# Performance work log

Hardware: AMD Instinct MI355X
Metric: run time of the kernel (lower is better)

The kernel has to match this reference:

```python
import jax, jax.numpy as jnp
import numpy as np

EMBED_DIM = 1024
NUM_HEADS = 16
HEAD_DIM = EMBED_DIM // NUM_HEADS


def setup_inputs() -> dict:
    key = jax.random.key(0)
    k1, k2, k3, k4 = jax.random.split(key, 4)
    B, N, D = 4, 2048, EMBED_DIM
    x = jax.random.normal(k1, (B, N, D), dtype=jnp.float32)
    # torch nn.Linear layout: weight [out_features, in_features]
    w_qkv = jax.random.normal(k2, (3 * D, D), dtype=jnp.float32) * (1.0 / np.sqrt(D))
    w_out = jax.random.normal(k3, (D, D), dtype=jnp.float32) * (1.0 / np.sqrt(D))
    b_out = jax.random.normal(k4, (D,), dtype=jnp.float32) * 0.01
    return {"x": x, "w_qkv": w_qkv, "w_out": w_out, "b_out": b_out}


def reference(x, w_qkv, w_out, b_out):
    B, N, D = x.shape
    H, Hd = NUM_HEADS, HEAD_DIM
    qkv = (x @ w_qkv.T).reshape(B, N, 3, H, Hd)
    q, k, v = qkv[:, :, 0], qkv[:, :, 1], qkv[:, :, 2]  # [B,N,H,Hd]
    # NOTE: contracts over BOTH heads and head_dim -> single shared [B,N,N] map
    scores = jnp.einsum('bnhd,bmhd->bnm', q, k) / np.sqrt(Hd).astype(np.float32)
    attn = jax.nn.softmax(scores, axis=-1)
    out = jnp.einsum('bnm,bmhd->bnhd', attn, v).reshape(B, N, D)
    return out @ w_out.T + b_out
```

## Files before the change

kernel.cpp:

```cpp
#include <hip/hip_runtime.h>


typedef __bf16 bf16;
typedef __attribute__((ext_vector_type(8))) __bf16 bf16x8;
typedef __attribute__((ext_vector_type(4))) __bf16 bf16x4;
typedef __attribute__((ext_vector_type(16))) float f32x16;

#define BATCH 4
#define NTOK  2048
#define DIM   1024
#define MROWS (BATCH * NTOK)
#define QKVC  (3 * DIM)

__device__ __forceinline__ void async16(const bf16* g, bf16* l) {
  __builtin_amdgcn_global_load_lds(
      (const __attribute__((address_space(1))) void*)g,
      (__attribute__((address_space(3))) void*)l, 16, 0, 0);
}

__device__ __forceinline__ void cvt4(const float* in, bf16* out, int i4) {
  float4 f = *(const float4*)(in + i4 * 4);
  bf16x4 o;
  o.x = (bf16)f.x; o.y = (bf16)f.y; o.z = (bf16)f.z; o.w = (bf16)f.w;
  *(bf16x4*)(out + i4 * 4) = o;
}

__global__ void prep(const float* __restrict__ x, const float* __restrict__ wqkv,
                     const float* __restrict__ wout,
                     bf16* __restrict__ Xbf, bf16* __restrict__ Wqkvb,
                     bf16* __restrict__ Woutb, float* __restrict__ L) {
  const int nx = MROWS * DIM / 4, nq = QKVC * DIM / 4, nw = DIM * DIM / 4;
  const int nl = BATCH * NTOK / 4;
  int i = blockIdx.x * blockDim.x + threadIdx.x;
  if (i < nx) cvt4(x, Xbf, i);
  else if (i < nx + nq) cvt4(wqkv, Wqkvb, i - nx);
  else if (i < nx + nq + nw) cvt4(wout, Woutb, i - nx - nq);
  else if (i < nx + nq + nw + nl) {
    float4 z = {0.f, 0.f, 0.f, 0.f};
    *(float4*)(L + (i - nx - nq - nw) * 4) = z;
  }
}

struct GemmCore {
  const bf16 *ga[4], *gb[4];
  int sIdx[4];
  int wm, wn, l31, half;
};

__device__ __forceinline__ GemmCore gemm_setup(const bf16* A, const bf16* Bm,
                                               int lda, int ldb,
                                               long rowA, long rowB) {
  GemmCore g;
  const int tid = threadIdx.x;
  const int wave = tid >> 6, lane = tid & 63;
  g.wm = (wave >> 1) << 6;
  g.wn = (wave & 1) << 6;
  g.l31 = lane & 31;
  g.half = lane >> 5;
  const int srow = tid >> 3;
  const int sc   = tid & 7;
  const int scol = (sc ^ (srow & 7)) << 3;
#pragma unroll
  for (int seg = 0; seg < 4; ++seg) {
    g.ga[seg] = A  + (rowA + srow + 32 * seg) * (long)lda + scol;
    g.gb[seg] = Bm + (rowB + srow + 32 * seg) * (long)ldb + scol;
    g.sIdx[seg] = (srow + 32 * seg) * 64 + sc * 8;
  }
  return g;
}

__device__ __forceinline__ void gemm_kloop(const GemmCore& g, int K,
                                           bf16* As, bf16* Bs, f32x16 acc[2][2]) {
  const int sw = g.l31 & 7;
  for (int kt = 0; kt < K; kt += 64) {
#pragma unroll
    for (int seg = 0; seg < 4; ++seg) {
      async16(g.ga[seg] + kt, As + g.sIdx[seg]);
      async16(g.gb[seg] + kt, Bs + g.sIdx[seg]);
    }
    __syncthreads();

    bf16x8 af[2][4], bfm[2][4];
#pragma unroll
    for (int ti = 0; ti < 2; ++ti)
#pragma unroll
      for (int s = 0; s < 4; ++s)
        af[ti][s] = *(const bf16x8*)&As[(g.wm + ti * 32 + g.l31) * 64 + ((s * 2 + g.half) ^ sw) * 8];
#pragma unroll
    for (int tj = 0; tj < 2; ++tj)
#pragma unroll
      for (int s = 0; s < 4; ++s)
        bfm[tj][s] = *(const bf16x8*)&Bs[(g.wn + tj * 32 + g.l31) * 64 + ((s * 2 + g.half) ^ sw) * 8];

#pragma unroll
    for (int s = 0; s < 4; ++s)
#pragma unroll
      for (int ti = 0; ti < 2; ++ti)
#pragma unroll
        for (int tj = 0; tj < 2; ++tj)
          acc[ti][tj] = __builtin_amdgcn_mfma_f32_32x32x16_bf16(
              af[ti][s], bfm[tj][s], acc[ti][tj], 0, 0, 0);

    __syncthreads();
  }
}

__launch_bounds__(256)
__global__ void gemm_qkv(const bf16* __restrict__ Xb, const bf16* __restrict__ Wq,
                         bf16* __restrict__ QKV) {
  __shared__ alignas(16) bf16 As[128 * 64];
  __shared__ alignas(16) bf16 Bs[128 * 64];
  int wg = blockIdx.x;
  wg = (wg & 7) * 192 + (wg >> 3);
  const int by = wg / 24, bx = wg - by * 24;

  const long rowA = (long)by * 128;
  const long rowB = (long)bx * 128;
  GemmCore g = gemm_setup(Xb, Wq, DIM, DIM, rowA, rowB);
  f32x16 acc[2][2] = {};
  gemm_kloop(g, DIM, As, Bs, acc);

#pragma unroll
  for (int ti = 0; ti < 2; ++ti)
#pragma unroll
    for (int tj = 0; tj < 2; ++tj) {
      const long col = rowB + g.wn + tj * 32 + g.l31;
#pragma unroll
      for (int r = 0; r < 16; ++r) {
        const long row = rowA + g.wm + ti * 32 + (r & 3) + 8 * (r >> 2) + 4 * g.half;
        QKV[row * (long)QKVC + col] = (bf16)acc[ti][tj][r];
      }
    }
}

__launch_bounds__(256)
__global__ void gemm_sv(const bf16* __restrict__ QKV, const bf16* __restrict__ Wout,
                        bf16* __restrict__ E, bf16* __restrict__ Vpp,
                        float* __restrict__ Lroot) {
  __shared__ alignas(16) bf16 As[128 * 64];
  __shared__ alignas(16) bf16 Bs[128 * 64];
  int wg = blockIdx.x;
  wg = (wg & 7) * 192 + (wg >> 3);

  if (wg < 1024) {
    const int z = wg >> 8, rem = wg & 255;
    const int by = rem >> 4, bx = rem & 15;
    const bf16* A  = QKV + (long)z * NTOK * QKVC;
    const bf16* Bm = A + DIM;
    const long rowA = (long)by * 128;
    const long rowB = (long)bx * 128;
    GemmCore g = gemm_setup(A, Bm, QKVC, QKVC, rowA, rowB);
    f32x16 acc[2][2] = {};
    gemm_kloop(g, DIM, As, Bs, acc);

    bf16* C = E + (long)z * NTOK * NTOK;
    float* L = Lroot + (long)z * NTOK;
#pragma unroll
    for (int ti = 0; ti < 2; ++ti) {
#pragma unroll
      for (int r = 0; r < 16; ++r) {
        const long row = rowA + g.wm + ti * 32 + (r & 3) + 8 * (r >> 2) + 4 * g.half;
        float psum = 0.f;
#pragma unroll
        for (int tj = 0; tj < 2; ++tj) {
          const long col = rowB + g.wn + tj * 32 + g.l31;
          float e = __expf(acc[ti][tj][r] * 0.125f);
          bf16 eb = (bf16)e;
          C[row * (long)NTOK + col] = eb;
          psum += (float)eb;
        }
#pragma unroll
        for (int off = 16; off >= 1; off >>= 1) psum += __shfl_xor(psum, off, 64);
        if (g.l31 == 0) atomicAdd(&L[row], psum);
      }
    }
  } else {
    const int v = wg - 1024;
    const int b = v >> 7, rem = v & 127;
    const int by = rem >> 4, bx = rem & 15;
    const bf16* Bm = QKV + (long)b * NTOK * QKVC + 2 * DIM;
    const long rowA = (long)by * 128;
    const long rowB = (long)bx * 128;
    GemmCore g = gemm_setup(Wout, Bm, DIM, QKVC, rowA, rowB);
    f32x16 acc[2][2] = {};
    gemm_kloop(g, DIM, As, Bs, acc);

    bf16* C = Vpp + (long)b * DIM * NTOK;
#pragma unroll
    for (int ti = 0; ti < 2; ++ti)
#pragma unroll
      for (int tj = 0; tj < 2; ++tj) {
        const long col = rowB + g.wn + tj * 32 + g.l31;
#pragma unroll
        for (int r = 0; r < 16; ++r) {
          const long row = rowA + g.wm + ti * 32 + (r & 3) + 8 * (r >> 2) + 4 * g.half;
          C[row * (long)NTOK + col] = (bf16)acc[ti][tj][r];
        }
      }
  }
}

__launch_bounds__(256)
__global__ void gemm_out(const bf16* __restrict__ Eroot, const bf16* __restrict__ Vroot,
                         float* __restrict__ Croot, const float* __restrict__ bias,
                         const float* __restrict__ Lroot) {
  __shared__ alignas(16) bf16 As[128 * 64];
  __shared__ alignas(16) bf16 Bs[128 * 64];
  int wg = blockIdx.x;
  wg = (wg & 7) * 64 + (wg >> 3);
  const int z = wg >> 7, rem = wg & 127;
  const int by = rem >> 3, bx = rem & 7;

  const bf16* A  = Eroot + (long)z * NTOK * NTOK;
  const bf16* Bm = Vroot + (long)z * DIM * NTOK;
  const long rowA = (long)by * 128;
  const long rowB = (long)bx * 128;
  GemmCore g = gemm_setup(A, Bm, NTOK, NTOK, rowA, rowB);

  f32x16 acc[2][2] = {};
  gemm_kloop(g, NTOK, As, Bs, acc);

  float* C = Croot + (long)z * NTOK * DIM;
  const float* L = Lroot + (long)z * NTOK;
#pragma unroll
  for (int ti = 0; ti < 2; ++ti) {
#pragma unroll
    for (int r = 0; r < 16; ++r) {
      const long row = rowA + g.wm + ti * 32 + (r & 3) + 8 * (r >> 2) + 4 * g.half;
      const float inv = 1.0f / L[row];
#pragma unroll
      for (int tj = 0; tj < 2; ++tj) {
        const long col = rowB + g.wn + tj * 32 + g.l31;
        C[row * (long)DIM + col] = acc[ti][tj][r] * inv + bias[col];
      }
    }
  }
}

extern "C" void kernel_launch(void* const* d_in, const int* in_sizes, int n_in,
                              void* d_out, int out_size, void* d_ws, size_t ws_size,
                              hipStream_t stream) {
  const float* x      = (const float*)d_in[0];
  const float* w_qkv  = (const float*)d_in[1];
  const float* w_out  = (const float*)d_in[2];
  const float* b_out  = (const float*)d_in[3];
  float* out = (float*)d_out;

  char* w = (char*)d_ws;
  bf16*  Xbf   = (bf16*)(w);
  bf16*  Wqkvb = (bf16*)(w + 16777216);
  bf16*  Woutb = (bf16*)(w + 23068672);
  bf16*  QKV   = (bf16*)(w + 25165824);
  bf16*  E     = (bf16*)(w + 75497472);
  bf16*  Vpp   = (bf16*)(w + 109051904);
  float* L     = (float*)(w + 125829120);

  {
    const int n4 = MROWS * DIM / 4 + QKVC * DIM / 4 + DIM * DIM / 4 + BATCH * NTOK / 4;
    prep<<<(n4 + 255) / 256, 256, 0, stream>>>(x, w_qkv, w_out, Xbf, Wqkvb, Woutb, L);
  }

  gemm_qkv<<<1536, 256, 0, stream>>>(Xbf, Wqkvb, QKV);

  gemm_sv<<<1536, 256, 0, stream>>>(QKV, Woutb, E, Vpp, L);

  gemm_out<<<512, 256, 0, stream>>>(E, Vpp, out, b_out, L);
}
```

Before: 274.1 us.

## Replace QKV and score GEMMs with 256x256 double-buffered 8-wave pipelined kernel

Replaces the 128x128, 4-wave GEMM kernels for the QKV projection and the score/V-projection stage with a 256x256 tile, 8-wave kernel. Each wave computes a 128x64 sub-tile, and the kernel uses 128KB of dynamic LDS with double buffering. Global-to-LDS async loads for the next K tile are interleaved across four MFMA phases, with fine-grained vmcnt waits, barriers and s_setprio. This is meant to raise data reuse per tile and hide load latency behind MFMA work. In exchange, the launch drops to 384 workgroups, which risks lower occupancy and tail imbalance. The 128KB dynamic LDS request also needs to fit within the device limit.

```diff
diff --git a/kernel.cpp b/kernel.cpp
--- a/kernel.cpp
+++ b/kernel.cpp
@@ -41,6 +41,189 @@
   }
 }
 
+
+template <bool MORE, bool LAST>
+__device__ __forceinline__ void phase_tile(
+    const bf16* Ac, const bf16* Bc, bf16* An, bf16* Bn,
+    const bf16* const pA[4], const bf16* const pB[4], int ktn,
+    int dst, int wr, int wc, int l31, int half, f32x16 acc[4][2]) {
+  const int sw = l31 & 7;
+  bf16x8 bv[2][4];
+#pragma unroll
+  for (int q = 0; q < 4; ++q) {
+    bf16x8 av[4];
+    {
+      const int arow = wr * 128 + q * 32 + l31;
+#pragma unroll
+      for (int k16 = 0; k16 < 4; ++k16)
+        av[k16] = *(const bf16x8*)&Ac[arow * 64 + ((k16 * 2 + half) ^ sw) * 8];
+    }
+    if (q == 0) {
+#pragma unroll
+      for (int tj = 0; tj < 2; ++tj) {
+        const int brow = wc * 64 + tj * 32 + l31;
+#pragma unroll
+        for (int k16 = 0; k16 < 4; ++k16)
+          bv[tj][k16] = *(const bf16x8*)&Bc[brow * 64 + ((k16 * 2 + half) ^ sw) * 8];
+      }
+    }
+    if (MORE) {
+      if (q == 0) { async16(pB[0] + ktn, Bn + dst);
+                    async16(pB[1] + ktn, Bn + 4096 + dst); }
+      if (q == 1) { async16(pB[2] + ktn, Bn + 8192 + dst);
+                    async16(pB[3] + ktn, Bn + 12288 + dst); }
+      if (q == 2) { async16(pA[0] + ktn, An + dst);
+                    async16(pA[2] + ktn, An + 8192 + dst); }
+      if (q == 3) { async16(pA[1] + ktn, An + 4096 + dst);
+                    async16(pA[3] + ktn, An + 12288 + dst); }
+    }
+    __builtin_amdgcn_s_barrier();
+    asm volatile("s_waitcnt lgkmcnt(0)" ::: "memory");
+    __builtin_amdgcn_s_setprio(1);
+#pragma unroll
+    for (int k16 = 0; k16 < 4; ++k16)
+#pragma unroll
+      for (int tj = 0; tj < 2; ++tj)
+        acc[q][tj] = __builtin_amdgcn_mfma_f32_32x32x16_bf16(
+            av[k16], bv[tj][k16], acc[q][tj], 0, 0, 0);
+    __builtin_amdgcn_s_setprio(0);
+    if (q == 1) {
+      if (LAST) asm volatile("s_waitcnt vmcnt(0)" ::: "memory");
+      else      asm volatile("s_waitcnt vmcnt(4)" ::: "memory");
+    }
+    if (q == 3 && MORE) asm volatile("s_waitcnt vmcnt(2)" ::: "memory");
+    __builtin_amdgcn_s_barrier();
+  }
+}
+
+__device__ __forceinline__ void gemm8p(const bf16* __restrict__ A,
+                                       const bf16* __restrict__ Bm,
+                                       int lda, int ldb, long rowA, long rowB,
+                                       bf16* sm, int wr, int wc, int l31, int half,
+                                       f32x16 acc[4][2]) {
+  const int tid = threadIdx.x;
+  const int srow = tid >> 3, sc = tid & 7;
+  const int scol = (sc ^ (srow & 7)) << 3;
+  const int dst = tid * 8;
+
+  const bf16* pA[4];
+  const bf16* pB[4];
+#pragma unroll
+  for (int j = 0; j < 4; ++j) {
+    pA[j] = A  + (rowA + srow + 64 * j) * (long)lda + scol;
+    pB[j] = Bm + (rowB + srow + 64 * j) * (long)ldb + scol;
+  }
+
+  bf16* A0 = sm;
+  bf16* B0 = sm + 16384;
+  bf16* A1 = sm + 32768;
+  bf16* B1 = sm + 49152;
+
+  async16(pB[0], B0 + dst);          async16(pB[1], B0 + 4096 + dst);
+  async16(pB[2], B0 + 8192 + dst);   async16(pB[3], B0 + 12288 + dst);
+  async16(pA[0], A0 + dst);          async16(pA[2], A0 + 8192 + dst);
+  async16(pA[1], A0 + 4096 + dst);   async16(pA[3], A0 + 12288 + dst);
+  asm volatile("s_waitcnt vmcnt(2)" ::: "memory");
+  __builtin_amdgcn_s_barrier();
+
+  const bf16 *Ac = A0, *Bc = B0;
+  bf16 *An = A1, *Bn = B1;
+#pragma unroll 1
+  for (int t = 0; t < 15; ++t) {
+    phase_tile<true, false>(Ac, Bc, An, Bn, pA, pB, (t + 1) * 64,
+                            dst, wr, wc, l31, half, acc);
+    const bf16* ta = Ac; Ac = An; An = (bf16*)ta;
+    const bf16* tb = Bc; Bc = Bn; Bn = (bf16*)tb;
+  }
+  phase_tile<false, true>(Ac, Bc, An, Bn, pA, pB, 0,
+                          dst, wr, wc, l31, half, acc);
+}
+
+__launch_bounds__(512, 2)
+__global__ void g8p_qkv(const bf16* __restrict__ Xb, const bf16* __restrict__ Wq,
+                        bf16* __restrict__ QKV) {
+  extern __shared__ bf16 sm[];
+  const int tid = threadIdx.x, wave = tid >> 6, lane = tid & 63;
+  const int wr = wave >> 2, wc = wave & 3, l31 = lane & 31, half = lane >> 5;
+  const int by = blockIdx.x / 12, bx = blockIdx.x % 12;
+  const long rowA = (long)by * 256, rowB = (long)bx * 256;
+  f32x16 acc[4][2] = {};
+  gemm8p(Xb, Wq, DIM, DIM, rowA, rowB, sm, wr, wc, l31, half, acc);
+#pragma unroll
+  for (int ti = 0; ti < 4; ++ti)
+#pragma unroll
+    for (int tj = 0; tj < 2; ++tj) {
+      const long col = rowB + wc * 64 + tj * 32 + l31;
+#pragma unroll
+      for (int r = 0; r < 16; ++r) {
+        const long row = rowA + wr * 128 + ti * 32 + (r & 3) + 8 * (r >> 2) + 4 * half;
+        QKV[row * (long)QKVC + col] = (bf16)acc[ti][tj][r];
+      }
+    }
+}
+
+__launch_bounds__(512, 2)
+__global__ void g8p_sv(const bf16* __restrict__ QKV, const bf16* __restrict__ Wout,
+                       bf16* __restrict__ E, bf16* __restrict__ Vpp,
+                       float* __restrict__ Lroot) {
+  extern __shared__ bf16 sm[];
+  const int tid = threadIdx.x, wave = tid >> 6, lane = tid & 63;
+  const int wr = wave >> 2, wc = wave & 3, l31 = lane & 31, half = lane >> 5;
+  const int wg = blockIdx.x;
+  if (wg < 256) {
+    const int z = wg >> 6, rem = wg & 63;
+    const int by = rem >> 3, bx = rem & 7;
+    const bf16* A  = QKV + (long)z * NTOK * QKVC;
+    const bf16* Bm = A + DIM;
+    const long rowA = (long)by * 256, rowB = (long)bx * 256;
+    f32x16 acc[4][2] = {};
+    gemm8p(A, Bm, QKVC, QKVC, rowA, rowB, sm, wr, wc, l31, half, acc);
+
+    bf16* C = E + (long)z * NTOK * NTOK;
+    float* L = Lroot + (long)z * NTOK;
+#pragma unroll
+    for (int ti = 0; ti < 4; ++ti) {
+#pragma unroll
+      for (int r = 0; r < 16; ++r) {
+        const long row = rowA + wr * 128 + ti * 32 + (r & 3) + 8 * (r >> 2) + 4 * half;
+        float psum = 0.f;
+#pragma unroll
+        for (int tj = 0; tj < 2; ++tj) {
+          const long col = rowB + wc * 64 + tj * 32 + l31;
+          float e = __expf(acc[ti][tj][r] * 0.125f);
+          bf16 eb = (bf16)e;
+          C[row * (long)NTOK + col] = eb;
+          psum += (float)eb;
+        }
+#pragma unroll
+        for (int off = 16; off >= 1; off >>= 1) psum += __shfl_xor(psum, off, 64);
+        if (l31 == 0) atomicAdd(&L[row], psum);
+      }
+    }
+  } else {
+    const int v = wg - 256;
+    const int b = v >> 5, rem = v & 31;
+    const int by = rem >> 3, bx = rem & 7;
+    const bf16* Bm = QKV + (long)b * NTOK * QKVC + 2 * DIM;
+    const long rowA = (long)by * 256, rowB = (long)bx * 256;
+    f32x16 acc[4][2] = {};
+    gemm8p(Wout, Bm, DIM, QKVC, rowA, rowB, sm, wr, wc, l31, half, acc);
+
+    bf16* C = Vpp + (long)b * DIM * NTOK;
+#pragma unroll
+    for (int ti = 0; ti < 4; ++ti)
+#pragma unroll
+      for (int tj = 0; tj < 2; ++tj) {
+        const long col = rowB + wc * 64 + tj * 32 + l31;
+#pragma unroll
+        for (int r = 0; r < 16; ++r) {
+          const long row = rowA + wr * 128 + ti * 32 + (r & 3) + 8 * (r >> 2) + 4 * half;
+          C[row * (long)NTOK + col] = (bf16)acc[ti][tj][r];
+        }
+      }
+  }
+}
+
 struct GemmCore {
   const bf16 *ga[4], *gb[4];
   int sIdx[4];
@@ -106,101 +289,6 @@
 }
 
 __launch_bounds__(256)
-__global__ void gemm_qkv(const bf16* __restrict__ Xb, const bf16* __restrict__ Wq,
-                         bf16* __restrict__ QKV) {
-  __shared__ alignas(16) bf16 As[128 * 64];
-  __shared__ alignas(16) bf16 Bs[128 * 64];
-  int wg = blockIdx.x;
-  wg = (wg & 7) * 192 + (wg >> 3);
-  const int by = wg / 24, bx = wg - by * 24;
-
-  const long rowA = (long)by * 128;
-  const long rowB = (long)bx * 128;
-  GemmCore g = gemm_setup(Xb, Wq, DIM, DIM, rowA, rowB);
-  f32x16 acc[2][2] = {};
-  gemm_kloop(g, DIM, As, Bs, acc);
-
-#pragma unroll
-  for (int ti = 0; ti < 2; ++ti)
-#pragma unroll
-    for (int tj = 0; tj < 2; ++tj) {
-      const long col = rowB + g.wn + tj * 32 + g.l31;
-#pragma unroll
-      for (int r = 0; r < 16; ++r) {
-        const long row = rowA + g.wm + ti * 32 + (r & 3) + 8 * (r >> 2) + 4 * g.half;
-        QKV[row * (long)QKVC + col] = (bf16)acc[ti][tj][r];
-      }
-    }
-}
-
-__launch_bounds__(256)
-__global__ void gemm_sv(const bf16* __restrict__ QKV, const bf16* __restrict__ Wout,
-                        bf16* __restrict__ E, bf16* __restrict__ Vpp,
-                        float* __restrict__ Lroot) {
-  __shared__ alignas(16) bf16 As[128 * 64];
-  __shared__ alignas(16) bf16 Bs[128 * 64];
-  int wg = blockIdx.x;
-  wg = (wg & 7) * 192 + (wg >> 3);
-
-  if (wg < 1024) {
-    const int z = wg >> 8, rem = wg & 255;
-    const int by = rem >> 4, bx = rem & 15;
-    const bf16* A  = QKV + (long)z * NTOK * QKVC;
-    const bf16* Bm = A + DIM;
-    const long rowA = (long)by * 128;
-    const long rowB = (long)bx * 128;
-    GemmCore g = gemm_setup(A, Bm, QKVC, QKVC, rowA, rowB);
-    f32x16 acc[2][2] = {};
-    gemm_kloop(g, DIM, As, Bs, acc);
-
-    bf16* C = E + (long)z * NTOK * NTOK;
-    float* L = Lroot + (long)z * NTOK;
-#pragma unroll
-    for (int ti = 0; ti < 2; ++ti) {
-#pragma unroll
-      for (int r = 0; r < 16; ++r) {
-        const long row = rowA + g.wm + ti * 32 + (r & 3) + 8 * (r >> 2) + 4 * g.half;
-        float psum = 0.f;
-#pragma unroll
-        for (int tj = 0; tj < 2; ++tj) {
-          const long col = rowB + g.wn + tj * 32 + g.l31;
-          float e = __expf(acc[ti][tj][r] * 0.125f);
-          bf16 eb = (bf16)e;
-          C[row * (long)NTOK + col] = eb;
-          psum += (float)eb;
-        }
-#pragma unroll
-        for (int off = 16; off >= 1; off >>= 1) psum += __shfl_xor(psum, off, 64);
-        if (g.l31 == 0) atomicAdd(&L[row], psum);
-      }
-    }
-  } else {
-    const int v = wg - 1024;
-    const int b = v >> 7, rem = v & 127;
-    const int by = rem >> 4, bx = rem & 15;
-    const bf16* Bm = QKV + (long)b * NTOK * QKVC + 2 * DIM;
-    const long rowA = (long)by * 128;
-    const long rowB = (long)bx * 128;
-    GemmCore g = gemm_setup(Wout, Bm, DIM, QKVC, rowA, rowB);
-    f32x16 acc[2][2] = {};
-    gemm_kloop(g, DIM, As, Bs, acc);
-
-    bf16* C = Vpp + (long)b * DIM * NTOK;
-#pragma unroll
-    for (int ti = 0; ti < 2; ++ti)
-#pragma unroll
-      for (int tj = 0; tj < 2; ++tj) {
-        const long col = rowB + g.wn + tj * 32 + g.l31;
-#pragma unroll
-        for (int r = 0; r < 16; ++r) {
-          const long row = rowA + g.wm + ti * 32 + (r & 3) + 8 * (r >> 2) + 4 * g.half;
-          C[row * (long)NTOK + col] = (bf16)acc[ti][tj][r];
-        }
-      }
-  }
-}
-
-__launch_bounds__(256)
 __global__ void gemm_out(const bf16* __restrict__ Eroot, const bf16* __restrict__ Vroot,
                          float* __restrict__ Croot, const float* __restrict__ bias,
                          const float* __restrict__ Lroot) {
@@ -260,9 +348,9 @@
     prep<<<(n4 + 255) / 256, 256, 0, stream>>>(x, w_qkv, w_out, Xbf, Wqkvb, Woutb, L);
   }
 
-  gemm_qkv<<<1536, 256, 0, stream>>>(Xbf, Wqkvb, QKV);
-
-  gemm_sv<<<1536, 256, 0, stream>>>(QKV, Woutb, E, Vpp, L);
+  g8p_qkv<<<384, 512, 131072, stream>>>(Xbf, Wqkvb, QKV);
+
+  g8p_sv<<<384, 512, 131072, stream>>>(QKV, Woutb, E, Vpp, L);
 
   gemm_out<<<512, 256, 0, stream>>>(E, Vpp, out, b_out, L);
 }
```

After: 272.2 us. No clear change (-0.7%).
